# Kernel optimization log

Measured on AMD Instinct MI355X. Metric: run time of the kernel, lower is better.

Reference implementation:

```python
import jax, jax.numpy as jnp
import numpy as np
from math import sqrt

P_DROP = 0.2  # dropout_rate

def setup_inputs() -> dict:
    key = jax.random.key(0)
    ks = jax.random.split(key, 5)
    B, Cin, H, W = 32, 128, 64, 64
    Cout, kh, kw = 256, 3, 3
    k = sqrt(1.0 / (Cin * kh * kw))  # He-style init std from module
    x = jax.random.normal(ks[0], (B, Cin, H, W), dtype=jnp.float32)
    weight = jax.random.normal(ks[1], (Cout, Cin, kh, kw), dtype=jnp.float32) * k
    bias = jax.random.normal(ks[2], (Cout,), dtype=jnp.float32) * k
    # uniforms used for torch.rand(...) > p per batch element ('w' mode draws fresh masks per sample)
    u_w = jax.random.uniform(ks[3], (B, Cout, Cin, kh, kw), dtype=jnp.float32)
    u_b = jax.random.uniform(ks[4], (B, Cout), dtype=jnp.float32)
    return {"x": x, "weight": weight, "bias": bias, "u_w": u_w, "u_b": u_b}

def reference(x, weight, bias, u_w, u_b):
    # 'w' mode: per-sample dropped-out weight/bias, conv per sample -> vmapped batched conv.
    # Note: mask is (rand > p) with NO 1/(1-p) rescaling, matching the torch code.
    w_mask = (u_w > P_DROP).astype(weight.dtype)          # [B,O,I,kh,kw]
    b_mask = (u_b > P_DROP).astype(bias.dtype)            # [B,O]
    w_per = weight[None] * w_mask                          # [B,O,I,kh,kw]
    b_per = bias[None] * b_mask                            # [B,O]

    def conv_one(xi, wi):  # xi: [Cin,H,W], wi: [O,I,kh,kw]
        return jax.lax.conv_general_dilated(
            xi[None], wi,
            window_strides=(1, 1),
            padding=((1, 1), (1, 1)),
            dimension_numbers=("NCHW", "OIHW", "NCHW"),
        )[0]

    y = jax.vmap(conv_one)(x, w_per)                       # [B,O,H,W]
    return y + b_per[:, :, None, None]
```

## Files before the change

kernel.cpp:

```cpp
#include <hip/hip_runtime.h>
#include <cstdint>
#include <cstddef>

#define CIN   128
#define COUT  256
#define HW    64
#define NSP   4096
#define KTOT  1152
#define BATCH 32
#define PDROP 0.2f
#define LDT   40

__device__ __forceinline__ unsigned short f2bf(float f) {
    unsigned int u = __builtin_bit_cast(unsigned int, f);
    u += 0x7fffu + ((u >> 16) & 1u);
    return (unsigned short)(u >> 16);
}

__device__ __align__(16) unsigned short g_zeros[64] = {0};

__device__ __forceinline__ void gl_lds16(const unsigned short* g, unsigned short* l) {
    __builtin_amdgcn_global_load_lds(
        (const __attribute__((address_space(1))) unsigned int*)g,
        (__attribute__((address_space(3))) unsigned int*)l,
        16, 0, 0);
}

__global__ __launch_bounds__(256) void prepass(
        const float* __restrict__ weight, const float* __restrict__ u_w,
        const float* __restrict__ x,
        unsigned short* __restrict__ wt, unsigned short* __restrict__ xt)
{
    __shared__ unsigned short sh[8704];
    const int t256 = threadIdx.x;

    if (blockIdx.x < 4096) {
        const int half = t256 >> 7;
        const int t    = t256 & 127;
        const int bo   = blockIdx.x * 2 + half;
        const int o    = bo & (COUT - 1);
        unsigned short* tile = sh + half * KTOT;
        const float4* wsrc = reinterpret_cast<const float4*>(weight + (size_t)o  * KTOT);
        const float4* usrc = reinterpret_cast<const float4*>(u_w    + (size_t)bo * KTOT);
        #pragma unroll
        for (int j = 0; j < 3; ++j) {
            const int idx = j * 128 + t;
            if (idx < KTOT / 4) {
                float4 wv = wsrc[idx];
                float4 uv = usrc[idx];
                const float w4[4] = {wv.x, wv.y, wv.z, wv.w};
                const float u4[4] = {uv.x, uv.y, uv.z, uv.w};
                #pragma unroll
                for (int c = 0; c < 4; ++c) {
                    const int ks = idx * 4 + c;
                    const int i  = ks / 9;
                    const int r  = ks - 9 * i;
                    tile[r * CIN + i] = f2bf((u4[c] > PDROP) ? w4[c] : 0.f);
                }
            }
        }
        __syncthreads();
        const uint4* src = reinterpret_cast<const uint4*>(tile);
        uint4* dst = reinterpret_cast<uint4*>(wt + (size_t)bo * KTOT);
        #pragma unroll
        for (int j = 0; j < 2; ++j) {
            const int idx = j * 128 + t;
            if (idx < KTOT / 8) dst[idx] = src[idx];
        }
    } else {
        const int bidx = blockIdx.x - 4096;
        const int b    = bidx >> 6;
        const int hw0  = (bidx & 63) * 64;
        const int ib   = t256 >> 4;
        const int hw4  = (t256 & 15) * 4;
        #pragma unroll
        for (int j = 0; j < 8; ++j) {
            const int i = ib + 16 * j;
            const float4 v = *reinterpret_cast<const float4*>(
                x + ((size_t)(b * CIN + i)) * NSP + hw0 + hw4);
            const float v4[4] = {v.x, v.y, v.z, v.w};
            #pragma unroll
            for (int c = 0; c < 4; ++c)
                sh[(hw4 + c) * 136 + i] = f2bf(v4[c]);
        }
        __syncthreads();
        #pragma unroll
        for (int j = 0; j < 4; ++j) {
            const int idx  = j * 256 + t256;
            const int row  = idx >> 4;
            const int part = idx & 15;
            const uint4 v = *reinterpret_cast<const uint4*>(&sh[row * 136 + part * 8]);
            *reinterpret_cast<uint4*>(
                xt + ((size_t)(b * NSP + hw0 + row)) * CIN + part * 8) = v;
        }
    }
}

__global__ __launch_bounds__(256, 3) void conv_v4(
        const unsigned short* __restrict__ wt,
        const unsigned short* __restrict__ xt,
        const float* __restrict__ bias, const float* __restrict__ u_b,
        float* __restrict__ out)
{
    using frag  = __attribute__((ext_vector_type(8))) short;
    using f32x4 = __attribute__((ext_vector_type(4))) float;

    __shared__ unsigned short Xs[4 * 66 * 64];
    __shared__ unsigned short As[128 * 64];

    const int tid  = threadIdx.x;
    const int lane = tid & 63;
    const int q    = lane >> 4;
    const int l15  = lane & 15;
    const int wv   = tid >> 6;
    const int wm   = (wv >> 1) * 64;
    const int wn   = (wv & 1) * 64;
    const int wnrow = wn >> 6;

    const int b   = blockIdx.z;
    const int m0  = blockIdx.y * 128;
    const int n0  = blockIdx.x * 128;
    const int ph0 = n0 >> 6;

    const unsigned short* wtb = wt + (size_t)(b * COUT + m0) * KTOT;
    const unsigned short* xtb = xt + (size_t)b * NSP * CIN;

    const int r8 = lane >> 3;
    const int p8 = lane & 7;
    const int cx = p8 ^ r8;
    const unsigned short* gA[4];
    unsigned short* ldsA[4];
    #pragma unroll
    for (int j = 0; j < 4; ++j) {
        const int row = wv * 32 + j * 8 + r8;
        gA[j]   = wtb + (size_t)row * KTOT + cx * 8;
        ldsA[j] = &As[(wv * 32 + j * 8) * 64];
    }

    const int kcl = (lane & 7) ^ ((1 + (lane >> 3)) & 7);
    const int xsrc_lane = (lane >> 3) * CIN + kcl * 8;
    const int hhx = ph0 - 1 + wv;
    const bool vrow = ((unsigned)hhx < 64u);
    unsigned short* const xdst = &Xs[(wv * 66 + 1) * 64];

    const int l7 = l15 & 7;
    const int physk0 = q ^ l7;
    const int physk1 = (4 + q) ^ l7;
    const int a_base = (wm + l15) * 64;
    int xoff[4];
    #pragma unroll
    for (int ni = 0; ni < 4; ++ni) xoff[ni] = (ni * 16 + l15 + 1) * 64;
    int xr[3][2];
    #pragma unroll
    for (int dxi = 0; dxi < 3; ++dxi)
        #pragma unroll
        for (int ki = 0; ki < 2; ++ki)
            xr[dxi][ki] = ((ki * 4 + q) ^ ((l15 + dxi) & 7)) * 8;

    f32x4 acc[4][4];
    #pragma unroll
    for (int i = 0; i < 4; ++i)
        #pragma unroll
        for (int j = 0; j < 4; ++j)
            acc[i][j] = (f32x4){0.f, 0.f, 0.f, 0.f};

    {
        const int cell = tid >> 5;
        const int rr   = cell >> 1;
        const int cc   = (cell & 1) ? 65 : 0;
        *reinterpret_cast<unsigned int*>(
            &Xs[(rr * 66 + cc) * 64 + (tid & 31) * 2]) = 0u;
    }

    #pragma unroll
    for (int s2 = 0; s2 < 2; ++s2) {
        const int i0 = s2 * 64;

        __syncthreads();

        {
            const unsigned short* sx = vrow
                ? xtb + (size_t)hhx * HW * CIN + i0 + xsrc_lane
                : g_zeros;
            #pragma unroll
            for (int g = 0; g < 8; ++g)
                gl_lds16(vrow ? (sx + g * 8 * CIN) : sx, xdst + g * 512);
        }

        #pragma unroll
        for (int tap = 0; tap < 9; ++tap) {
            const int dy  = tap / 3 - 1;
            const int dx  = tap - 3 * (tap / 3) - 1;
            const int dxi = dx + 1;

            if (tap) __syncthreads();

            const int k0 = tap * 128 + i0;
            #pragma unroll
            for (int j = 0; j < 4; ++j)
                gl_lds16(gA[j] + k0, ldsA[j]);

            __syncthreads();

            const int cb = (wnrow + dy + 1) * 4224 + dx * 64;

            #pragma unroll
            for (int ki = 0; ki < 2; ++ki) {
                const int pk = ki ? physk1 : physk0;
                frag af[4], bfr[4];
                #pragma unroll
                for (int mi = 0; mi < 4; ++mi)
                    af[mi] = *reinterpret_cast<const frag*>(
                        &As[a_base + mi * 1024 + pk * 8]);
                #pragma unroll
                for (int ni = 0; ni < 4; ++ni)
                    bfr[ni] = *reinterpret_cast<const frag*>(
                        &Xs[cb + xoff[ni] + xr[dxi][ki]]);
                #pragma unroll
                for (int mi = 0; mi < 4; ++mi)
                    #pragma unroll
                    for (int ni = 0; ni < 4; ++ni)
                        acc[mi][ni] = __builtin_amdgcn_mfma_f32_16x16x32_bf16(
                            af[mi], bfr[ni], acc[mi][ni], 0, 0, 0);
            }
        }
    }

    float* ob = out + (size_t)b * COUT * NSP;
    #pragma unroll
    for (int mi = 0; mi < 4; ++mi) {
        #pragma unroll
        for (int rg = 0; rg < 4; ++rg) {
            const int o  = m0 + wm + mi * 16 + q * 4 + rg;
            const float bvv = (u_b[b * COUT + o] > PDROP) ? bias[o] : 0.f;
            float* orow = ob + (size_t)o * NSP + n0 + wn + l15;
            #pragma unroll
            for (int ni = 0; ni < 4; ++ni)
                orow[ni * 16] = acc[mi][ni][rg] + bvv;
        }
    }
}

template<bool USE_WS>
__global__ __launch_bounds__(256) void conv_fb(
        const float* __restrict__ x, const float* __restrict__ weight,
        const float* __restrict__ bias, const float* __restrict__ u_w,
        const float* __restrict__ u_b, const unsigned short* __restrict__ wt,
        float* __restrict__ out)
{
    using frag  = __attribute__((ext_vector_type(8))) short;
    using f32x4 = __attribute__((ext_vector_type(4))) float;

    __shared__ unsigned short As[128 * LDT];
    __shared__ unsigned short Bs[128 * LDT];

    const int tid  = threadIdx.x;
    const int lane = tid & 63;
    const int q    = lane >> 4;
    const int l15  = lane & 15;
    const int wv   = tid >> 6;
    const int wm   = (wv >> 1) * 64;
    const int wn   = (wv & 1) * 64;

    const int b  = blockIdx.z;
    const int m0 = blockIdx.y * 128;
    const int n0 = blockIdx.x * 128;

    const int arow = tid >> 1;
    const int acol = (tid & 1) * 16;
    const int pn = tid & 127;
    const int kh = (tid >> 7) * 16;
    const int p  = n0 + pn;
    const int ph = p >> 6;
    const int pw = p & 63;

    const float* xb = x + (size_t)b * CIN * NSP;

    f32x4 acc[4][4];
    #pragma unroll
    for (int i = 0; i < 4; ++i)
        #pragma unroll
        for (int j = 0; j < 4; ++j)
            acc[i][j] = (f32x4){0.f, 0.f, 0.f, 0.f};

    const int a_rd = (wm + l15) * LDT + q * 8;
    const int b_rd = (wn + l15) * LDT + q * 8;

    for (int s = 0; s < 36; ++s) {
        const int r  = s >> 2;
        const int i0 = (s & 3) * 32;
        const int k0 = s * 32;

        uint4 av0, av1;
        float aw[16], au[16];
        if (USE_WS) {
            const uint4* src = reinterpret_cast<const uint4*>(
                wt + ((size_t)(b * COUT + m0 + arow)) * KTOT + k0 + acol);
            av0 = src[0];
            av1 = src[1];
        } else {
            const float* wsrc = weight + (size_t)(m0 + arow) * KTOT;
            const float* usrc = u_w + (size_t)(b * COUT + m0 + arow) * KTOT;
            #pragma unroll
            for (int ii = 0; ii < 16; ++ii) {
                const int kk = (i0 + acol + ii) * 9 + r;
                aw[ii] = wsrc[kk];
                au[ii] = usrc[kk];
            }
        }

        const int hh = ph + (r / 3) - 1;
        const int ww = pw + (r % 3) - 1;
        float bx[16];
        #pragma unroll
        for (int j = 0; j < 16; ++j) bx[j] = 0.f;
        if (((unsigned)hh < 64u) && ((unsigned)ww < 64u)) {
            const float* xsrc = xb + (size_t)(i0 + kh) * NSP + hh * HW + ww;
            #pragma unroll
            for (int j = 0; j < 16; ++j) bx[j] = xsrc[(size_t)j * NSP];
        }

        __syncthreads();

        if (USE_WS) {
            uint4* d = reinterpret_cast<uint4*>(&As[arow * LDT + acol]);
            d[0] = av0; d[1] = av1;
        } else {
            union { unsigned short u16[16]; uint4 v[2]; } tu;
            #pragma unroll
            for (int ii = 0; ii < 16; ++ii)
                tu.u16[ii] = f2bf((au[ii] > PDROP) ? aw[ii] : 0.f);
            uint4* d = reinterpret_cast<uint4*>(&As[arow * LDT + acol]);
            d[0] = tu.v[0]; d[1] = tu.v[1];
        }
        {
            union { unsigned short u16[16]; uint4 v[2]; } tu;
            #pragma unroll
            for (int j = 0; j < 16; ++j) tu.u16[j] = f2bf(bx[j]);
            uint4* d = reinterpret_cast<uint4*>(&Bs[pn * LDT + kh]);
            d[0] = tu.v[0]; d[1] = tu.v[1];
        }

        __syncthreads();

        frag af[4], bfr[4];
        #pragma unroll
        for (int mi = 0; mi < 4; ++mi)
            af[mi] = *reinterpret_cast<const frag*>(&As[a_rd + mi * 16 * LDT]);
        #pragma unroll
        for (int ni = 0; ni < 4; ++ni)
            bfr[ni] = *reinterpret_cast<const frag*>(&Bs[b_rd + ni * 16 * LDT]);
        #pragma unroll
        for (int mi = 0; mi < 4; ++mi)
            #pragma unroll
            for (int ni = 0; ni < 4; ++ni)
                acc[mi][ni] = __builtin_amdgcn_mfma_f32_16x16x32_bf16(
                    af[mi], bfr[ni], acc[mi][ni], 0, 0, 0);
    }

    float* ob = out + (size_t)b * COUT * NSP;
    #pragma unroll
    for (int mi = 0; mi < 4; ++mi) {
        #pragma unroll
        for (int rg = 0; rg < 4; ++rg) {
            const int o = m0 + wm + mi * 16 + q * 4 + rg;
            const float bvv = (u_b[b * COUT + o] > PDROP) ? bias[o] : 0.f;
            float* orow = ob + (size_t)o * NSP + n0 + wn + l15;
            #pragma unroll
            for (int ni = 0; ni < 4; ++ni)
                orow[ni * 16] = acc[mi][ni][rg] + bvv;
        }
    }
}

extern "C" void kernel_launch(void* const* d_in, const int* in_sizes, int n_in,
                              void* d_out, int out_size, void* d_ws, size_t ws_size,
                              hipStream_t stream)
{
    const float* x      = (const float*)d_in[0];
    const float* weight = (const float*)d_in[1];
    const float* bias   = (const float*)d_in[2];
    const float* u_w    = (const float*)d_in[3];
    const float* u_b    = (const float*)d_in[4];
    float* out = (float*)d_out;

    const size_t wt_bytes = (size_t)BATCH * COUT * KTOT * sizeof(unsigned short);
    const size_t xt_bytes = (size_t)BATCH * NSP * CIN * sizeof(unsigned short);
    dim3 grid(NSP / 128, COUT / 128, BATCH);

    if (ws_size >= wt_bytes + xt_bytes) {
        unsigned short* wtp = (unsigned short*)d_ws;
        unsigned short* xtp = (unsigned short*)((char*)d_ws + wt_bytes);
        prepass<<<4096 + 2048, 256, 0, stream>>>(weight, u_w, x, wtp, xtp);
        conv_v4<<<grid, 256, 0, stream>>>(wtp, xtp, bias, u_b, out);
    } else if (ws_size >= wt_bytes) {
        unsigned short* wtp = (unsigned short*)d_ws;
        prepass<<<4096, 256, 0, stream>>>(weight, u_w, x, wtp, nullptr);
        conv_fb<true><<<grid, 256, 0, stream>>>(x, weight, bias, u_w, u_b, wtp, out);
    } else {
        conv_fb<false><<<grid, 256, 0, stream>>>(x, weight, bias, u_w, u_b, nullptr, out);
    }
}
```

Baseline: 284.1 us.

## Pre-swizzle weights into MFMA fragment layout and load A directly from global

The prepass now writes the masked bf16 weights in a per-tap, per-slab layout that matches the MFMA A-fragment order. This lets the conv kernel read A fragments straight from global memory (through the cache) instead of staging them in LDS. That removes the A shared buffer and the two barriers per tap. The cost is that A comes from global/L2 with non-LDS latency on every MFMA step, and the prepass launches fewer, larger blocks. The intermediate-workspace fallback path is dropped.

```diff
diff --git a/kernel.cpp b/kernel.cpp
--- a/kernel.cpp
+++ b/kernel.cpp
@@ -29,50 +29,64 @@
 __global__ __launch_bounds__(256) void prepass(
         const float* __restrict__ weight, const float* __restrict__ u_w,
         const float* __restrict__ x,
-        unsigned short* __restrict__ wt, unsigned short* __restrict__ xt)
+        unsigned short* __restrict__ wt2, unsigned short* __restrict__ xt)
 {
-    __shared__ unsigned short sh[8704];
-    const int t256 = threadIdx.x;
-
-    if (blockIdx.x < 4096) {
-        const int half = t256 >> 7;
-        const int t    = t256 & 127;
-        const int bo   = blockIdx.x * 2 + half;
-        const int o    = bo & (COUT - 1);
-        unsigned short* tile = sh + half * KTOT;
-        const float4* wsrc = reinterpret_cast<const float4*>(weight + (size_t)o  * KTOT);
-        const float4* usrc = reinterpret_cast<const float4*>(u_w    + (size_t)bo * KTOT);
-        #pragma unroll
-        for (int j = 0; j < 3; ++j) {
-            const int idx = j * 128 + t;
-            if (idx < KTOT / 4) {
-                float4 wv = wsrc[idx];
-                float4 uv = usrc[idx];
-                const float w4[4] = {wv.x, wv.y, wv.z, wv.w};
-                const float u4[4] = {uv.x, uv.y, uv.z, uv.w};
-                #pragma unroll
-                for (int c = 0; c < 4; ++c) {
-                    const int ks = idx * 4 + c;
-                    const int i  = ks / 9;
-                    const int r  = ks - 9 * i;
-                    tile[r * CIN + i] = f2bf((u4[c] > PDROP) ? w4[c] : 0.f);
-                }
+    __shared__ unsigned short sh[9280];
+    const int t = threadIdx.x;
+
+    if (blockIdx.x < 1024) {
+        const int bw = blockIdx.x;
+        const int rg = bw & 15;
+        const int mt = (bw >> 4) & 1;
+        const int b  = bw >> 5;
+        const int o0 = mt * 128 + rg * 8;
+
+        #pragma unroll
+        for (int j = 0; j < 9; ++j) {
+            const int idx = j * 256 + t;
+            const int bo_loc = idx / 288;
+            const int rem    = idx - bo_loc * 288;
+            const int o  = o0 + bo_loc;
+            const float4 wv = reinterpret_cast<const float4*>(
+                weight + (size_t)o * KTOT)[rem];
+            const float4 uv = reinterpret_cast<const float4*>(
+                u_w + (size_t)(b * COUT + o) * KTOT)[rem];
+            const float w4[4] = {wv.x, wv.y, wv.z, wv.w};
+            const float u4[4] = {uv.x, uv.y, uv.z, uv.w};
+            #pragma unroll
+            for (int c = 0; c < 4; ++c) {
+                const int ks  = rem * 4 + c;
+                const int i   = ks / 9;
+                const int tap = ks - 9 * i;
+                sh[bo_loc * 1160 + tap * CIN + i] =
+                    f2bf((u4[c] > PDROP) ? w4[c] : 0.f);
             }
         }
         __syncthreads();
-        const uint4* src = reinterpret_cast<const uint4*>(tile);
-        uint4* dst = reinterpret_cast<uint4*>(wt + (size_t)bo * KTOT);
-        #pragma unroll
-        for (int j = 0; j < 2; ++j) {
-            const int idx = j * 128 + t;
-            if (idx < KTOT / 8) dst[idx] = src[idx];
+
+        unsigned short* dstb = wt2 + ((size_t)(b * 2 + mt) * 18) * 8192;
+        #pragma unroll
+        for (int j = 0; j < 5; ++j) {
+            const int g = j * 256 + t;
+            if (g < 1152) {
+                const int row_loc = g & 7;
+                const int tsc     = g >> 3;
+                const int tap   = tsc >> 4;
+                const int slab  = (tsc >> 3) & 1;
+                const int chunk = tsc & 7;
+                const uint4 v = *reinterpret_cast<const uint4*>(
+                    &sh[row_loc * 1160 + tap * CIN + slab * 64 + chunk * 8]);
+                *reinterpret_cast<uint4*>(
+                    dstb + (size_t)(tap * 2 + slab) * 8192 + chunk * 1024
+                         + (rg * 8 + row_loc) * 8) = v;
+            }
         }
     } else {
-        const int bidx = blockIdx.x - 4096;
+        const int bidx = blockIdx.x - 1024;
         const int b    = bidx >> 6;
         const int hw0  = (bidx & 63) * 64;
-        const int ib   = t256 >> 4;
-        const int hw4  = (t256 & 15) * 4;
+        const int ib   = t >> 4;
+        const int hw4  = (t & 15) * 4;
         #pragma unroll
         for (int j = 0; j < 8; ++j) {
             const int i = ib + 16 * j;
@@ -86,7 +100,7 @@
         __syncthreads();
         #pragma unroll
         for (int j = 0; j < 4; ++j) {
-            const int idx  = j * 256 + t256;
+            const int idx  = j * 256 + t;
             const int row  = idx >> 4;
             const int part = idx & 15;
             const uint4 v = *reinterpret_cast<const uint4*>(&sh[row * 136 + part * 8]);
@@ -96,8 +110,8 @@
     }
 }
 
-__global__ __launch_bounds__(256, 3) void conv_v4(
-        const unsigned short* __restrict__ wt,
+__global__ __launch_bounds__(256, 3) void conv_v5(
+        const unsigned short* __restrict__ wt2,
         const unsigned short* __restrict__ xt,
         const float* __restrict__ bias, const float* __restrict__ u_b,
         float* __restrict__ out)
@@ -106,7 +120,6 @@
     using f32x4 = __attribute__((ext_vector_type(4))) float;
 
     __shared__ unsigned short Xs[4 * 66 * 64];
-    __shared__ unsigned short As[128 * 64];
 
     const int tid  = threadIdx.x;
     const int lane = tid & 63;
@@ -122,20 +135,11 @@
     const int n0  = blockIdx.x * 128;
     const int ph0 = n0 >> 6;
 
-    const unsigned short* wtb = wt + (size_t)(b * COUT + m0) * KTOT;
     const unsigned short* xtb = xt + (size_t)b * NSP * CIN;
 
-    const int r8 = lane >> 3;
-    const int p8 = lane & 7;
-    const int cx = p8 ^ r8;
-    const unsigned short* gA[4];
-    unsigned short* ldsA[4];
-    #pragma unroll
-    for (int j = 0; j < 4; ++j) {
-        const int row = wv * 32 + j * 8 + r8;
-        gA[j]   = wtb + (size_t)row * KTOT + cx * 8;
-        ldsA[j] = &As[(wv * 32 + j * 8) * 64];
-    }
+    const unsigned short* a_bm = wt2
+        + (size_t)(b * 2 + (m0 >> 7)) * 147456
+        + (size_t)(wm + l15) * 8 + q * 1024;
 
     const int kcl = (lane & 7) ^ ((1 + (lane >> 3)) & 7);
     const int xsrc_lane = (lane >> 3) * CIN + kcl * 8;
@@ -143,10 +147,6 @@
     const bool vrow = ((unsigned)hhx < 64u);
     unsigned short* const xdst = &Xs[(wv * 66 + 1) * 64];
 
-    const int l7 = l15 & 7;
-    const int physk0 = q ^ l7;
-    const int physk1 = (4 + q) ^ l7;
-    const int a_base = (wm + l15) * 64;
     int xoff[4];
     #pragma unroll
     for (int ni = 0; ni < 4; ++ni) xoff[ni] = (ni * 16 + l15 + 1) * 64;
@@ -187,31 +187,23 @@
                 gl_lds16(vrow ? (sx + g * 8 * CIN) : sx, xdst + g * 512);
         }
 
+        __syncthreads();
+
         #pragma unroll
         for (int tap = 0; tap < 9; ++tap) {
             const int dy  = tap / 3 - 1;
             const int dx  = tap - 3 * (tap / 3) - 1;
             const int dxi = dx + 1;
-
-            if (tap) __syncthreads();
-
-            const int k0 = tap * 128 + i0;
-            #pragma unroll
-            for (int j = 0; j < 4; ++j)
-                gl_lds16(gA[j] + k0, ldsA[j]);
-
-            __syncthreads();
-
+            const unsigned short* at = a_bm + (size_t)(tap * 2 + s2) * 8192;
             const int cb = (wnrow + dy + 1) * 4224 + dx * 64;
 
             #pragma unroll
             for (int ki = 0; ki < 2; ++ki) {
-                const int pk = ki ? physk1 : physk0;
                 frag af[4], bfr[4];
                 #pragma unroll
                 for (int mi = 0; mi < 4; ++mi)
                     af[mi] = *reinterpret_cast<const frag*>(
-                        &As[a_base + mi * 1024 + pk * 8]);
+                        at + ki * 4096 + mi * 128);
                 #pragma unroll
                 for (int ni = 0; ni < 4; ++ni)
                     bfr[ni] = *reinterpret_cast<const frag*>(
@@ -241,12 +233,10 @@
     }
 }
 
-template<bool USE_WS>
 __global__ __launch_bounds__(256) void conv_fb(
         const float* __restrict__ x, const float* __restrict__ weight,
         const float* __restrict__ bias, const float* __restrict__ u_w,
-        const float* __restrict__ u_b, const unsigned short* __restrict__ wt,
-        float* __restrict__ out)
+        const float* __restrict__ u_b, float* __restrict__ out)
 {
     using frag  = __attribute__((ext_vector_type(8))) short;
     using f32x4 = __attribute__((ext_vector_type(4))) float;
@@ -289,16 +279,9 @@
     for (int s = 0; s < 36; ++s) {
         const int r  = s >> 2;
         const int i0 = (s & 3) * 32;
-        const int k0 = s * 32;
-
-        uint4 av0, av1;
+
         float aw[16], au[16];
-        if (USE_WS) {
-            const uint4* src = reinterpret_cast<const uint4*>(
-                wt + ((size_t)(b * COUT + m0 + arow)) * KTOT + k0 + acol);
-            av0 = src[0];
-            av1 = src[1];
-        } else {
+        {
             const float* wsrc = weight + (size_t)(m0 + arow) * KTOT;
             const float* usrc = u_w + (size_t)(b * COUT + m0 + arow) * KTOT;
             #pragma unroll
@@ -322,10 +305,7 @@
 
         __syncthreads();
 
-        if (USE_WS) {
-            uint4* d = reinterpret_cast<uint4*>(&As[arow * LDT + acol]);
-            d[0] = av0; d[1] = av1;
-        } else {
+        {
             union { unsigned short u16[16]; uint4 v[2]; } tu;
             #pragma unroll
             for (int ii = 0; ii < 16; ++ii)
@@ -391,13 +371,9 @@
     if (ws_size >= wt_bytes + xt_bytes) {
         unsigned short* wtp = (unsigned short*)d_ws;
         unsigned short* xtp = (unsigned short*)((char*)d_ws + wt_bytes);
-        prepass<<<4096 + 2048, 256, 0, stream>>>(weight, u_w, x, wtp, xtp);
-        conv_v4<<<grid, 256, 0, stream>>>(wtp, xtp, bias, u_b, out);
-    } else if (ws_size >= wt_bytes) {
-        unsigned short* wtp = (unsigned short*)d_ws;
-        prepass<<<4096, 256, 0, stream>>>(weight, u_w, x, wtp, nullptr);
-        conv_fb<true><<<grid, 256, 0, stream>>>(x, weight, bias, u_w, u_b, wtp, out);
+        prepass<<<1024 + 2048, 256, 0, stream>>>(weight, u_w, x, wtp, xtp);
+        conv_v5<<<grid, 256, 0, stream>>>(wtp, xtp, bias, u_b, out);
     } else {
-        conv_fb<false><<<grid, 256, 0, stream>>>(x, weight, bias, u_w, u_b, nullptr, out);
-    }
-}
+        conv_fb<<<grid, 256, 0, stream>>>(x, weight, bias, u_w, u_b, out);
+    }
+}
```

Result: slower. 297.7 us (+4.8%).
